# Performance work log

Hardware: AMD Instinct MI355X
Metric: run time of the kernel (lower is better)

The kernel has to match this reference:

```python
import jax, jax.numpy as jnp
import numpy as np

OBS, HID, LAT = 1024, 2048, 256
VOCAB, HQ = 8192, 4
COMMIT = 0.5
N = 16384
LN_EPS = 1e-5


def setup_inputs() -> dict:
    key = jax.random.key(0)
    ks = jax.random.split(key, 7)

    def lin_w(k, fan_in, shape):
        # torch nn.Linear default init: U(-1/sqrt(fan_in), 1/sqrt(fan_in))
        bound = 1.0 / np.sqrt(fan_in)
        return jax.random.uniform(k, shape, jnp.float32, -bound, bound)

    return {
        "x": jax.random.normal(ks[0], (N, OBS), jnp.float32),
        # embeddings initialized uniform(-0.5, 0.5) as in the module
        "codebooks": jax.random.uniform(ks[1], (HQ, VOCAB, LAT), jnp.float32, -0.5, 0.5),
        "enc_w1": lin_w(ks[2], OBS, (OBS, HID)),
        "enc_b1": jnp.zeros((HID,), jnp.float32),
        "ln_g": jnp.ones((HID,), jnp.float32),
        "ln_b": jnp.zeros((HID,), jnp.float32),
        "enc_w2": lin_w(ks[3], HID, (HID, LAT)),
        "enc_b2": jnp.zeros((LAT,), jnp.float32),
        "dec_w1": lin_w(ks[4], LAT, (LAT, HID)),
        "dec_b1": jnp.zeros((HID,), jnp.float32),
        "dec_w2": lin_w(ks[5], HID, (HID, OBS)),
        "dec_b2": jnp.zeros((OBS,), jnp.float32),
    }


def reference(x, codebooks, enc_w1, enc_b1, ln_g, ln_b, enc_w2, enc_b2,
              dec_w1, dec_b1, dec_w2, dec_b2):
    sg = jax.lax.stop_gradient
    # encoder: Linear -> LayerNorm -> ReLU -> Linear
    h = x @ enc_w1 + enc_b1                      # [N, HID]
    mu = h.mean(-1, keepdims=True)
    var = ((h - mu) ** 2).mean(-1, keepdims=True)  # biased var, matches torch LN
    h = (h - mu) * jax.lax.rsqrt(var + LN_EPS) * ln_g + ln_b
    h = jax.nn.relu(h)
    latent = h @ enc_w2 + enc_b2                 # [N, LAT]

    total = jnp.float32(0.0)
    resid = latent
    code_sum = jnp.zeros_like(latent)
    for l in range(HQ):
        E = codebooks[l]                         # [VOCAB, LAT]
        # squared euclidean distances (argmin identical to cdist argmin)
        d2 = ((resid * resid).sum(-1, keepdims=True)
              - 2.0 * (resid @ E.T)
              + (E * E).sum(-1))                 # [N, VOCAB]
        idx = jnp.argmin(d2, axis=-1)            # [N]
        q = E[idx]                               # [N, LAT] gather
        codebook_loss = jnp.mean((q - sg(resid)) ** 2)
        commit_loss = jnp.mean((sg(q) - resid) ** 2)
        total = total + codebook_loss + COMMIT * commit_loss
        code_sum = code_sum + q
        resid = resid - q

    # straight-through estimator
    quant = latent + sg(code_sum - latent)
    # decoder: Linear -> ReLU -> Linear
    dh = jax.nn.relu(quant @ dec_w1 + dec_b1)
    recon = dh @ dec_w2 + dec_b2                 # [N, OBS]
    total = total + 0.5 * jnp.mean((recon - x) ** 2)
    return total
```

## Files before the change

### kernel.cpp

```cpp
#include <hip/hip_runtime.h>

#define N_ROWS 16384
#define OBS    1024
#define HID    2048
#define LAT    256
#define VOCAB  8192
#define HQ     4
#define LN_EPS 1e-5f

typedef unsigned short u16;
typedef unsigned long long u64;
typedef __bf16 bf16x8 __attribute__((ext_vector_type(8)));
typedef float  f32x4  __attribute__((ext_vector_type(4)));

static __device__ __forceinline__ unsigned int float_to_ordered(float f) {
    unsigned int u = __float_as_uint(f);
    return (u & 0x80000000u) ? ~u : (u | 0x80000000u);
}
static __device__ __forceinline__ u16 f2bf(float f) {
    unsigned int u = __float_as_uint(f);
    unsigned int r = u + 0x7FFFu + ((u >> 16) & 1u);
    return (u16)(r >> 16);
}
static __device__ __forceinline__ float bf2f(u16 u) {
    return __uint_as_float((unsigned int)u << 16);
}

#define GL2LDS(gp, lp) __builtin_amdgcn_global_load_lds( \
    (const __attribute__((address_space(1))) void*)(gp), \
    (__attribute__((address_space(3))) void*)(lp), 16, 0, 0)

template<int EPI>
__global__ __launch_bounds__(256, 4) void mfma_gemm_k(
    const u16* __restrict__ Abf, const u16* __restrict__ Bbf,
    const float* __restrict__ bias,
    u16* __restrict__ Cbf,
    float* __restrict__ lat, float* __restrict__ resid, u16* __restrict__ rbf,
    const float* __restrict__ X, double* __restrict__ lacc,
    int K, int Nd)
{
    __shared__ u16 As[128 * 64];
    __shared__ u16 Bs[128 * 64];

    const int tid  = threadIdx.x;
    const int wv   = tid >> 6, lane = tid & 63;
    const int wm   = wv & 1,   wn   = wv >> 1;
    const int m_   = lane & 15, g   = lane >> 4;
    const int m0   = blockIdx.x * 128;
    const int n0   = blockIdx.y * 128;

    f32x4 acc[4][4];
#pragma unroll
    for (int i = 0; i < 4; ++i)
#pragma unroll
        for (int j = 0; j < 4; ++j)
            acc[i][j] = f32x4{0.f, 0.f, 0.f, 0.f};

    const u16* Ablk = Abf + (size_t)m0 * K;
    const u16* Bblk = Bbf + (size_t)n0 * K;

    for (int k0 = 0; k0 < K; k0 += 64) {
#pragma unroll
        for (int c = 0; c < 4; ++c) {
            const int ci = (wv * 4 + c) * 64 + lane;
            const int r  = ci >> 3;
            const int cc = ci & 7;
            const int kc = (cc ^ (r & 7)) << 3;
            GL2LDS(Ablk + (size_t)r * K + k0 + kc, As + (wv * 4 + c) * 512);
            GL2LDS(Bblk + (size_t)r * K + k0 + kc, Bs + (wv * 4 + c) * 512);
        }
        __syncthreads();
#pragma unroll
        for (int ks = 0; ks < 2; ++ks) {
            const int ccw = ks * 4 + g;
            const int sw  = (ccw ^ (m_ & 7)) << 3;
            bf16x8 af[4], bfr[4];
#pragma unroll
            for (int t = 0; t < 4; ++t) {
                af[t]  = *(const bf16x8*)&As[(wm * 64 + t * 16 + m_) * 64 + sw];
                bfr[t] = *(const bf16x8*)&Bs[(wn * 64 + t * 16 + m_) * 64 + sw];
            }
#pragma unroll
            for (int mi = 0; mi < 4; ++mi)
#pragma unroll
                for (int ni = 0; ni < 4; ++ni)
                    acc[mi][ni] = __builtin_amdgcn_mfma_f32_16x16x32_bf16(
                        af[mi], bfr[ni], acc[mi][ni], 0, 0, 0);
        }
        __syncthreads();
    }

    float bs[4];
#pragma unroll
    for (int ni = 0; ni < 4; ++ni) bs[ni] = bias[n0 + wn * 64 + ni * 16 + m_];

    if constexpr (EPI == 3) {
        float lsum = 0.f;
#pragma unroll
        for (int mi = 0; mi < 4; ++mi)
#pragma unroll
            for (int j = 0; j < 4; ++j) {
                const int row = m0 + wm * 64 + mi * 16 + g * 4 + j;
#pragma unroll
                for (int ni = 0; ni < 4; ++ni) {
                    const int col = n0 + wn * 64 + ni * 16 + m_;
                    float r = acc[mi][ni][j] + bs[ni] - X[(size_t)row * Nd + col];
                    lsum = fmaf(r, r, lsum);
                }
            }
#pragma unroll
        for (int off = 32; off >= 1; off >>= 1) lsum += __shfl_xor(lsum, off);
        __shared__ float red[4];
        if (lane == 0) red[wv] = lsum;
        __syncthreads();
        if (tid == 0)
            atomicAdd(lacc, (double)(red[0] + red[1] + red[2] + red[3]));
    } else {
#pragma unroll
        for (int mi = 0; mi < 4; ++mi)
#pragma unroll
            for (int j = 0; j < 4; ++j) {
                const int row = m0 + wm * 64 + mi * 16 + g * 4 + j;
#pragma unroll
                for (int ni = 0; ni < 4; ++ni) {
                    const int col = n0 + wn * 64 + ni * 16 + m_;
                    float v = acc[mi][ni][j] + bs[ni];
                    if constexpr (EPI == 1) v = fmaxf(v, 0.f);
                    if constexpr (EPI == 2) {
                        lat  [(size_t)row * Nd + col] = v;
                        resid[(size_t)row * Nd + col] = v;
                        rbf  [(size_t)row * Nd + col] = f2bf(v);
                    } else {
                        Cbf[(size_t)row * Nd + col] = f2bf(v);
                    }
                }
            }
    }
}

__global__ __launch_bounds__(256) void tpose_bf_k(
    const float* __restrict__ W, u16* __restrict__ Wt, int K, int N)
{
    __shared__ u16 t[32][33];
    const int lx = threadIdx.x & 31, ly = threadIdx.x >> 5;
    const int n0 = blockIdx.x * 32, k0 = blockIdx.y * 32;
#pragma unroll
    for (int i = 0; i < 4; ++i)
        t[ly + 8 * i][lx] = f2bf(W[(size_t)(k0 + ly + 8 * i) * N + n0 + lx]);
    __syncthreads();
#pragma unroll
    for (int i = 0; i < 4; ++i)
        Wt[(size_t)(n0 + ly + 8 * i) * K + k0 + lx] = t[lx][ly + 8 * i];
}

__device__ __forceinline__ float block_reduce_bcast(float v, float* scratch) {
#pragma unroll
    for (int off = 32; off >= 1; off >>= 1) v += __shfl_xor(v, off);
    const int tid = threadIdx.x;
    __syncthreads();
    if ((tid & 63) == 0) scratch[tid >> 6] = v;
    __syncthreads();
    return scratch[0] + scratch[1] + scratch[2] + scratch[3];
}

__global__ __launch_bounds__(256) void ln_relu_bf_k(
    u16* __restrict__ h, const float* __restrict__ g, const float* __restrict__ b)
{
    __shared__ float scratch[4];
    const int tid = threadIdx.x;
    u16* hp = h + (size_t)blockIdx.x * HID + tid * 8;

    ushort4 r0 = *(const ushort4*)hp;
    ushort4 r1 = *(const ushort4*)(hp + 4);
    float v[8] = {bf2f(r0.x), bf2f(r0.y), bf2f(r0.z), bf2f(r0.w),
                  bf2f(r1.x), bf2f(r1.y), bf2f(r1.z), bf2f(r1.w)};

    float s = 0.f;
#pragma unroll
    for (int e = 0; e < 8; ++e) s += v[e];
    const float mu = block_reduce_bcast(s, scratch) * (1.f / HID);

    float vs = 0.f;
#pragma unroll
    for (int e = 0; e < 8; ++e) { float d = v[e] - mu; vs = fmaf(d, d, vs); }
    const float var = block_reduce_bcast(vs, scratch) * (1.f / HID);
    const float rs = rsqrtf(var + LN_EPS);

    ushort4 o0, o1;
#pragma unroll
    for (int e = 0; e < 8; ++e) {
        const int col = tid * 8 + e;
        float w = (v[e] - mu) * rs * g[col] + b[col];
        w = fmaxf(w, 0.f);
        u16 bb = f2bf(w);
        if (e < 4) ((u16*)&o0)[e] = bb; else ((u16*)&o1)[e - 4] = bb;
    }
    *(ushort4*)hp = o0;
    *(ushort4*)(hp + 4) = o1;
}

__global__ __launch_bounds__(256) void enorm_k(
    const float* __restrict__ cb, float* __restrict__ enorm,
    u64* __restrict__ keys, double* __restrict__ accs)
{
    if (blockIdx.x < 64) keys[blockIdx.x * 256 + threadIdx.x] = ~0ull;
    if (blockIdx.x == 64 && threadIdx.x < 2) accs[threadIdx.x] = 0.0;
    const int row  = blockIdx.x * 4 + (threadIdx.x >> 6);
    const int lane = threadIdx.x & 63;
    float4 v = *(const float4*)(cb + (size_t)row * LAT + lane * 4);
    float s = v.x * v.x + v.y * v.y + v.z * v.z + v.w * v.w;
#pragma unroll
    for (int off = 32; off >= 1; off >>= 1) s += __shfl_xor(s, off);
    if (lane == 0) enorm[row] = s;
}

__global__ __launch_bounds__(256) void f2bf_k(
    const float* __restrict__ in, u16* __restrict__ out)
{
    size_t i = ((size_t)blockIdx.x * 256 + threadIdx.x) * 4;
    float4 v = *(const float4*)(in + i);
    ushort4 o;
    o.x = f2bf(v.x); o.y = f2bf(v.y); o.z = f2bf(v.z); o.w = f2bf(v.w);
    *(ushort4*)(out + i) = o;
}

__global__ __launch_bounds__(256) void f2bf_neg2_k(
    const float* __restrict__ in, u16* __restrict__ out)
{
    size_t i = ((size_t)blockIdx.x * 256 + threadIdx.x) * 4;
    float4 v = *(const float4*)(in + i);
    ushort4 o;
    o.x = f2bf(-2.f * v.x); o.y = f2bf(-2.f * v.y);
    o.z = f2bf(-2.f * v.z); o.w = f2bf(-2.f * v.w);
    *(ushort4*)(out + i) = o;
}

__global__ __launch_bounds__(256, 4) void dist_mfma_k(
    const u16* __restrict__ Abf, const u16* __restrict__ Bneg2,
    const float* __restrict__ enorm, u64* __restrict__ keys)
{
    __shared__ u16 As[128 * 64];
    __shared__ u16 Bs[128 * 64];
    __shared__ u64 shk[128][2];

    const int tid  = threadIdx.x;
    const int wv   = tid >> 6, lane = tid & 63;
    const int wm   = wv & 1,   wn   = wv >> 1;
    const int m_   = lane & 15, g   = lane >> 4;
    const int m0   = blockIdx.x * 128;
    const int n0   = blockIdx.y * 128;

    f32x4 acc[4][4];
#pragma unroll
    for (int ni = 0; ni < 4; ++ni) {
        const float en = enorm[n0 + wn * 64 + ni * 16 + m_];
#pragma unroll
        for (int mi = 0; mi < 4; ++mi)
            acc[mi][ni] = f32x4{en, en, en, en};
    }

    const u16* Ablk = Abf   + (size_t)m0 * LAT;
    const u16* Bblk = Bneg2 + (size_t)n0 * LAT;

    for (int k0 = 0; k0 < LAT; k0 += 64) {
#pragma unroll
        for (int c = 0; c < 4; ++c) {
            const int ci = (wv * 4 + c) * 64 + lane;
            const int r  = ci >> 3;
            const int cc = ci & 7;
            const int kc = (cc ^ (r & 7)) << 3;
            GL2LDS(Ablk + (size_t)r * LAT + k0 + kc, As + (wv * 4 + c) * 512);
            GL2LDS(Bblk + (size_t)r * LAT + k0 + kc, Bs + (wv * 4 + c) * 512);
        }
        __syncthreads();
#pragma unroll
        for (int ks = 0; ks < 2; ++ks) {
            const int ccw = ks * 4 + g;
            const int sw  = (ccw ^ (m_ & 7)) << 3;
            bf16x8 af[4], bfr[4];
#pragma unroll
            for (int t = 0; t < 4; ++t) {
                af[t]  = *(const bf16x8*)&As[(wm * 64 + t * 16 + m_) * 64 + sw];
                bfr[t] = *(const bf16x8*)&Bs[(wn * 64 + t * 16 + m_) * 64 + sw];
            }
#pragma unroll
            for (int mi = 0; mi < 4; ++mi)
#pragma unroll
                for (int ni = 0; ni < 4; ++ni)
                    acc[mi][ni] = __builtin_amdgcn_mfma_f32_16x16x32_bf16(
                        af[mi], bfr[ni], acc[mi][ni], 0, 0, 0);
        }
        __syncthreads();
    }

#pragma unroll
    for (int mi = 0; mi < 4; ++mi)
#pragma unroll
        for (int j = 0; j < 4; ++j) {
            float bs_ = acc[mi][0][j];
            int   bi_ = n0 + wn * 64 + m_;
#pragma unroll
            for (int ni = 1; ni < 4; ++ni) {
                const float s = acc[mi][ni][j];
                const int   v = n0 + wn * 64 + ni * 16 + m_;
                if (s < bs_) { bs_ = s; bi_ = v; }
            }
            u64 best = ((u64)float_to_ordered(bs_) << 32) | (unsigned)bi_;
#pragma unroll
            for (int mask = 1; mask <= 8; mask <<= 1) {
                u64 o = __shfl_xor(best, mask);
                best = o < best ? o : best;
            }
            if (m_ == 0) shk[wm * 64 + mi * 16 + g * 4 + j][wn] = best;
        }
    __syncthreads();
    if (tid < 128) {
        u64 a = shk[tid][0], b = shk[tid][1];
        atomicMin(&keys[m0 + tid], a < b ? a : b);
    }
}

template<bool LAST>
__global__ __launch_bounds__(256) void vq_update_k(
    float* __restrict__ resid, u16* __restrict__ aux,
    const float* __restrict__ latent,
    const float* __restrict__ E,
    u64* __restrict__ keys, double* __restrict__ acc)
{
    __shared__ float red[4];
    const int tid = threadIdx.x;
    const int base = blockIdx.x * 16;
    float lsum = 0.f;
    for (int r = 0; r < 16; ++r) {
        const int row = base + r;
        const int idx = (int)(keys[row] & 0xFFFFFFFFull);
        const float q = E[(size_t)idx * LAT + tid];
        float v = resid[(size_t)row * LAT + tid] - q;
        if constexpr (LAST) {
            aux[(size_t)row * LAT + tid] =
                f2bf(latent[(size_t)row * LAT + tid] - v);
        } else {
            resid[(size_t)row * LAT + tid] = v;
            aux[(size_t)row * LAT + tid] = f2bf(v);
        }
        lsum = fmaf(v, v, lsum);
    }
    if (!LAST && tid < 16) keys[base + tid] = ~0ull;
#pragma unroll
    for (int off = 32; off >= 1; off >>= 1) lsum += __shfl_xor(lsum, off);
    if ((tid & 63) == 0) red[tid >> 6] = lsum;
    __syncthreads();
    if (tid == 0) atomicAdd(acc, (double)(red[0] + red[1] + red[2] + red[3]));
}

__global__ void finalize_k(const double* __restrict__ acc, float* __restrict__ out) {
    double total = 1.5 * acc[0] / (double)((size_t)N_ROWS * LAT)
                 + 0.5 * acc[1] / (double)((size_t)N_ROWS * OBS);
    out[0] = (float)total;
}

extern "C" void kernel_launch(void* const* d_in, const int* in_sizes, int n_in,
                              void* d_out, int out_size, void* d_ws, size_t ws_size,
                              hipStream_t stream)
{
    const float* x      = (const float*)d_in[0];
    const float* cb     = (const float*)d_in[1];
    const float* enc_w1 = (const float*)d_in[2];
    const float* enc_b1 = (const float*)d_in[3];
    const float* ln_g   = (const float*)d_in[4];
    const float* ln_b   = (const float*)d_in[5];
    const float* enc_w2 = (const float*)d_in[6];
    const float* enc_b2 = (const float*)d_in[7];
    const float* dec_w1 = (const float*)d_in[8];
    const float* dec_b1 = (const float*)d_in[9];
    const float* dec_w2 = (const float*)d_in[10];
    const float* dec_b2 = (const float*)d_in[11];

    char* ws = (char*)d_ws;
    const size_t MB = 1ull << 20;
    u16* hbuf = (u16*)ws;
    u16* xbf = (u16*)(ws + 64 * MB);
    u16* cbb = (u16*)(ws + 64 * MB);
    u16* rbf = (u16*)(ws + 80 * MB);
    u16* qbf = (u16*)(ws + 88 * MB);
    float* latent = (float*)(ws + 96 * MB);
    float* resid  = (float*)(ws + 112 * MB);
    u16* w1T  = (u16*)(ws + 128 * MB);
    u16* w2T  = (u16*)(ws + 132 * MB);
    u16* wd1T = (u16*)(ws + 133 * MB);
    u16* wd2T = (u16*)(ws + 134 * MB);
    float* enorm = (float*)(ws + 138 * MB);
    u64*   keys  = (u64*)(ws + 138 * MB + 131072);
    double* accs = (double*)(ws + 138 * MB + 262144);

    enorm_k<<<HQ * VOCAB / 4, 256, 0, stream>>>(cb, enorm, keys, accs);

    tpose_bf_k<<<dim3(HID / 32, OBS / 32), 256, 0, stream>>>(enc_w1, w1T, OBS, HID);
    tpose_bf_k<<<dim3(LAT / 32, HID / 32), 256, 0, stream>>>(enc_w2, w2T, HID, LAT);
    tpose_bf_k<<<dim3(HID / 32, LAT / 32), 256, 0, stream>>>(dec_w1, wd1T, LAT, HID);
    tpose_bf_k<<<dim3(OBS / 32, HID / 32), 256, 0, stream>>>(dec_w2, wd2T, HID, OBS);
    f2bf_k<<<(int)((size_t)N_ROWS * OBS / 1024), 256, 0, stream>>>(x, xbf);

    mfma_gemm_k<0><<<dim3(N_ROWS / 128, HID / 128), 256, 0, stream>>>(
        xbf, w1T, enc_b1, hbuf, nullptr, nullptr, nullptr, nullptr, nullptr, OBS, HID);
    ln_relu_bf_k<<<N_ROWS, 256, 0, stream>>>(hbuf, ln_g, ln_b);
    mfma_gemm_k<2><<<dim3(N_ROWS / 128, LAT / 128), 256, 0, stream>>>(
        hbuf, w2T, enc_b2, nullptr, latent, resid, rbf, nullptr, nullptr, HID, LAT);

    f2bf_neg2_k<<<(int)((size_t)HQ * VOCAB * LAT / 1024), 256, 0, stream>>>(cb, cbb);

    for (int l = 0; l < HQ; ++l) {
        dist_mfma_k<<<dim3(N_ROWS / 128, VOCAB / 128), 256, 0, stream>>>(
            rbf, cbb + (size_t)l * VOCAB * LAT, enorm + (size_t)l * VOCAB, keys);
        if (l < HQ - 1)
            vq_update_k<false><<<N_ROWS / 16, 256, 0, stream>>>(
                resid, rbf, nullptr, cb + (size_t)l * VOCAB * LAT, keys, accs);
        else
            vq_update_k<true><<<N_ROWS / 16, 256, 0, stream>>>(
                resid, qbf, latent, cb + (size_t)l * VOCAB * LAT, keys, accs);
    }

    mfma_gemm_k<1><<<dim3(N_ROWS / 128, HID / 128), 256, 0, stream>>>(
        qbf, wd1T, dec_b1, hbuf, nullptr, nullptr, nullptr, nullptr, nullptr, LAT, HID);
    mfma_gemm_k<3><<<dim3(N_ROWS / 128, OBS / 128), 256, 0, stream>>>(
        hbuf, wd2T, dec_b2, nullptr, nullptr, nullptr, nullptr, x, accs + 1, HID, OBS);

    finalize_k<<<1, 1, 0, stream>>>(accs, (float*)d_out);
}
```

Measured before the change: 898.9 us.

## Keep distance A-fragments in registers, double-buffer codebook tiles, retile latent GEMM

```diff
diff --git a/kernel.cpp b/kernel.cpp
--- a/kernel.cpp
+++ b/kernel.cpp
@@ -35,7 +35,6 @@
     const u16* __restrict__ Abf, const u16* __restrict__ Bbf,
     const float* __restrict__ bias,
     u16* __restrict__ Cbf,
-    float* __restrict__ lat, float* __restrict__ resid, u16* __restrict__ rbf,
     const float* __restrict__ X, double* __restrict__ lacc,
     int K, int Nd)
 {
@@ -126,16 +125,82 @@
                     const int col = n0 + wn * 64 + ni * 16 + m_;
                     float v = acc[mi][ni][j] + bs[ni];
                     if constexpr (EPI == 1) v = fmaxf(v, 0.f);
-                    if constexpr (EPI == 2) {
-                        lat  [(size_t)row * Nd + col] = v;
-                        resid[(size_t)row * Nd + col] = v;
-                        rbf  [(size_t)row * Nd + col] = f2bf(v);
-                    } else {
-                        Cbf[(size_t)row * Nd + col] = f2bf(v);
-                    }
+                    Cbf[(size_t)row * Nd + col] = f2bf(v);
                 }
             }
     }
+}
+
+__global__ __launch_bounds__(256, 4) void gemm2_k(
+    const u16* __restrict__ Abf, const u16* __restrict__ Bbf,
+    const float* __restrict__ bias,
+    float* __restrict__ lat, float* __restrict__ resid, u16* __restrict__ rbf)
+{
+    __shared__ u16 As[64 * 64];
+    __shared__ u16 Bs[64 * 64];
+
+    const int tid = threadIdx.x;
+    const int wv  = tid >> 6, lane = tid & 63;
+    const int wm  = wv & 1,   wn   = wv >> 1;
+    const int m_  = lane & 15, g   = lane >> 4;
+    const int m0  = blockIdx.x * 64;
+    const int n0  = blockIdx.y * 64;
+
+    f32x4 acc[2][2];
+#pragma unroll
+    for (int i = 0; i < 2; ++i)
+#pragma unroll
+        for (int j = 0; j < 2; ++j)
+            acc[i][j] = f32x4{0.f, 0.f, 0.f, 0.f};
+
+    const u16* Ablk = Abf + (size_t)m0 * HID;
+    const u16* Bblk = Bbf + (size_t)n0 * HID;
+
+    for (int k0 = 0; k0 < HID; k0 += 64) {
+#pragma unroll
+        for (int c = 0; c < 2; ++c) {
+            const int ci = (wv * 2 + c) * 64 + lane;
+            const int r  = ci >> 3;
+            const int cc = ci & 7;
+            const int kc = (cc ^ (r & 7)) << 3;
+            GL2LDS(Ablk + (size_t)r * HID + k0 + kc, As + (wv * 2 + c) * 512);
+            GL2LDS(Bblk + (size_t)r * HID + k0 + kc, Bs + (wv * 2 + c) * 512);
+        }
+        __syncthreads();
+#pragma unroll
+        for (int ks = 0; ks < 2; ++ks) {
+            const int ccw = ks * 4 + g;
+            const int sw  = (ccw ^ (m_ & 7)) << 3;
+            bf16x8 af[2], bfr[2];
+#pragma unroll
+            for (int t = 0; t < 2; ++t) {
+                af[t]  = *(const bf16x8*)&As[(wm * 32 + t * 16 + m_) * 64 + sw];
+                bfr[t] = *(const bf16x8*)&Bs[(wn * 32 + t * 16 + m_) * 64 + sw];
+            }
+#pragma unroll
+            for (int mi = 0; mi < 2; ++mi)
+#pragma unroll
+                for (int ni = 0; ni < 2; ++ni)
+                    acc[mi][ni] = __builtin_amdgcn_mfma_f32_16x16x32_bf16(
+                        af[mi], bfr[ni], acc[mi][ni], 0, 0, 0);
+        }
+        __syncthreads();
+    }
+
+#pragma unroll
+    for (int mi = 0; mi < 2; ++mi)
+#pragma unroll
+        for (int j = 0; j < 4; ++j) {
+            const int row = m0 + wm * 32 + mi * 16 + g * 4 + j;
+#pragma unroll
+            for (int ni = 0; ni < 2; ++ni) {
+                const int col = n0 + wn * 32 + ni * 16 + m_;
+                float v = acc[mi][ni][j] + bias[col];
+                lat  [(size_t)row * LAT + col] = v;
+                resid[(size_t)row * LAT + col] = v;
+                rbf  [(size_t)row * LAT + col] = f2bf(v);
+            }
+        }
 }
 
 __global__ __launch_bounds__(256) void tpose_bf_k(
@@ -201,16 +266,21 @@
 
 __global__ __launch_bounds__(256) void enorm_k(
     const float* __restrict__ cb, float* __restrict__ enorm,
-    u64* __restrict__ keys, double* __restrict__ accs)
+    u16* __restrict__ cbb, u64* __restrict__ keys, double* __restrict__ accs)
 {
     if (blockIdx.x < 64) keys[blockIdx.x * 256 + threadIdx.x] = ~0ull;
     if (blockIdx.x == 64 && threadIdx.x < 2) accs[threadIdx.x] = 0.0;
     const int row  = blockIdx.x * 4 + (threadIdx.x >> 6);
     const int lane = threadIdx.x & 63;
-    float4 v = *(const float4*)(cb + (size_t)row * LAT + lane * 4);
+    const size_t off = (size_t)row * LAT + lane * 4;
+    float4 v = *(const float4*)(cb + off);
+    ushort4 o;
+    o.x = f2bf(-2.f * v.x); o.y = f2bf(-2.f * v.y);
+    o.z = f2bf(-2.f * v.z); o.w = f2bf(-2.f * v.w);
+    *(ushort4*)(cbb + off) = o;
     float s = v.x * v.x + v.y * v.y + v.z * v.z + v.w * v.w;
 #pragma unroll
-    for (int off = 32; off >= 1; off >>= 1) s += __shfl_xor(s, off);
+    for (int off2 = 32; off2 >= 1; off2 >>= 1) s += __shfl_xor(s, off2);
     if (lane == 0) enorm[row] = s;
 }
 
@@ -224,85 +294,94 @@
     *(ushort4*)(out + i) = o;
 }
 
-__global__ __launch_bounds__(256) void f2bf_neg2_k(
-    const float* __restrict__ in, u16* __restrict__ out)
-{
-    size_t i = ((size_t)blockIdx.x * 256 + threadIdx.x) * 4;
-    float4 v = *(const float4*)(in + i);
-    ushort4 o;
-    o.x = f2bf(-2.f * v.x); o.y = f2bf(-2.f * v.y);
-    o.z = f2bf(-2.f * v.z); o.w = f2bf(-2.f * v.w);
-    *(ushort4*)(out + i) = o;
-}
-
-__global__ __launch_bounds__(256, 4) void dist_mfma_k(
+__global__ __launch_bounds__(256, 3) void dist_mfma_k(
     const u16* __restrict__ Abf, const u16* __restrict__ Bneg2,
     const float* __restrict__ enorm, u64* __restrict__ keys)
 {
-    __shared__ u16 As[128 * 64];
-    __shared__ u16 Bs[128 * 64];
-    __shared__ u64 shk[128][2];
-
-    const int tid  = threadIdx.x;
-    const int wv   = tid >> 6, lane = tid & 63;
-    const int wm   = wv & 1,   wn   = wv >> 1;
-    const int m_   = lane & 15, g   = lane >> 4;
-    const int m0   = blockIdx.x * 128;
-    const int n0   = blockIdx.y * 128;
-
-    f32x4 acc[4][4];
-#pragma unroll
-    for (int ni = 0; ni < 4; ++ni) {
-        const float en = enorm[n0 + wn * 64 + ni * 16 + m_];
-#pragma unroll
-        for (int mi = 0; mi < 4; ++mi)
-            acc[mi][ni] = f32x4{en, en, en, en};
-    }
-
-    const u16* Ablk = Abf   + (size_t)m0 * LAT;
+    __shared__ u16 Bs[2][128 * 64];
+
+    const int tid = threadIdx.x;
+    const int wv  = tid >> 6, lane = tid & 63;
+    const int m_  = lane & 15, g   = lane >> 4;
+    const int m0  = blockIdx.x * 128;
+    const int n0  = blockIdx.y * 128;
+
+    bf16x8 af[2][8];
+    const u16* Arow = Abf + (size_t)(m0 + wv * 32 + m_) * LAT + g * 8;
+#pragma unroll
+    for (int mi = 0; mi < 2; ++mi)
+#pragma unroll
+        for (int kb = 0; kb < 8; ++kb)
+            af[mi][kb] = *(const bf16x8*)(Arow + mi * 16 * LAT + kb * 32);
+
+    f32x4 acc[2][8];
+#pragma unroll
+    for (int ni = 0; ni < 8; ++ni) {
+        const float en = enorm[n0 + ni * 16 + m_];
+        acc[0][ni] = f32x4{en, en, en, en};
+        acc[1][ni] = f32x4{en, en, en, en};
+    }
+
     const u16* Bblk = Bneg2 + (size_t)n0 * LAT;
-
-    for (int k0 = 0; k0 < LAT; k0 += 64) {
-#pragma unroll
-        for (int c = 0; c < 4; ++c) {
-            const int ci = (wv * 4 + c) * 64 + lane;
-            const int r  = ci >> 3;
-            const int cc = ci & 7;
-            const int kc = (cc ^ (r & 7)) << 3;
-            GL2LDS(Ablk + (size_t)r * LAT + k0 + kc, As + (wv * 4 + c) * 512);
-            GL2LDS(Bblk + (size_t)r * LAT + k0 + kc, Bs + (wv * 4 + c) * 512);
-        }
+#pragma unroll
+    for (int c = 0; c < 4; ++c) {
+        const int ci = (wv * 4 + c) * 64 + lane;
+        const int r  = ci >> 3;
+        const int cc = ci & 7;
+        const int kc = (cc ^ (r & 7)) << 3;
+        GL2LDS(Bblk + (size_t)r * LAT + kc, &Bs[0][(wv * 4 + c) * 512]);
+    }
+
+#pragma unroll
+    for (int k0i = 0; k0i < 4; ++k0i) {
         __syncthreads();
+        if (k0i < 3) {
+            const int k0n = (k0i + 1) * 64;
+#pragma unroll
+            for (int c = 0; c < 4; ++c) {
+                const int ci = (wv * 4 + c) * 64 + lane;
+                const int r  = ci >> 3;
+                const int cc = ci & 7;
+                const int kc = (cc ^ (r & 7)) << 3;
+                GL2LDS(Bblk + (size_t)r * LAT + k0n + kc,
+                       &Bs[(k0i + 1) & 1][(wv * 4 + c) * 512]);
+            }
+        }
+        const u16* bsc = Bs[k0i & 1];
 #pragma unroll
         for (int ks = 0; ks < 2; ++ks) {
+            const int kb  = k0i * 2 + ks;
             const int ccw = ks * 4 + g;
             const int sw  = (ccw ^ (m_ & 7)) << 3;
-            bf16x8 af[4], bfr[4];
-#pragma unroll
-            for (int t = 0; t < 4; ++t) {
-                af[t]  = *(const bf16x8*)&As[(wm * 64 + t * 16 + m_) * 64 + sw];
-                bfr[t] = *(const bf16x8*)&Bs[(wn * 64 + t * 16 + m_) * 64 + sw];
-            }
-#pragma unroll
-            for (int mi = 0; mi < 4; ++mi)
-#pragma unroll
-                for (int ni = 0; ni < 4; ++ni)
-                    acc[mi][ni] = __builtin_amdgcn_mfma_f32_16x16x32_bf16(
-                        af[mi], bfr[ni], acc[mi][ni], 0, 0, 0);
-        }
-        __syncthreads();
-    }
-
-#pragma unroll
-    for (int mi = 0; mi < 4; ++mi)
+#pragma unroll
+            for (int nn = 0; nn < 2; ++nn) {
+                bf16x8 bfr[4];
+#pragma unroll
+                for (int q = 0; q < 4; ++q) {
+                    const int row = (nn * 4 + q) * 16 + m_;
+                    bfr[q] = *(const bf16x8*)&bsc[row * 64 + sw];
+                }
+#pragma unroll
+                for (int mi = 0; mi < 2; ++mi)
+#pragma unroll
+                    for (int q = 0; q < 4; ++q)
+                        acc[mi][nn * 4 + q] =
+                            __builtin_amdgcn_mfma_f32_16x16x32_bf16(
+                                af[mi][kb], bfr[q], acc[mi][nn * 4 + q], 0, 0, 0);
+            }
+        }
+    }
+
+#pragma unroll
+    for (int mi = 0; mi < 2; ++mi)
 #pragma unroll
         for (int j = 0; j < 4; ++j) {
             float bs_ = acc[mi][0][j];
-            int   bi_ = n0 + wn * 64 + m_;
-#pragma unroll
-            for (int ni = 1; ni < 4; ++ni) {
+            int   bi_ = n0 + m_;
+#pragma unroll
+            for (int ni = 1; ni < 8; ++ni) {
                 const float s = acc[mi][ni][j];
-                const int   v = n0 + wn * 64 + ni * 16 + m_;
+                const int   v = n0 + ni * 16 + m_;
                 if (s < bs_) { bs_ = s; bi_ = v; }
             }
             u64 best = ((u64)float_to_ordered(bs_) << 32) | (unsigned)bi_;
@@ -311,13 +390,9 @@
                 u64 o = __shfl_xor(best, mask);
                 best = o < best ? o : best;
             }
-            if (m_ == 0) shk[wm * 64 + mi * 16 + g * 4 + j][wn] = best;
-        }
-    __syncthreads();
-    if (tid < 128) {
-        u64 a = shk[tid][0], b = shk[tid][1];
-        atomicMin(&keys[m0 + tid], a < b ? a : b);
-    }
+            if (m_ == 0)
+                atomicMin(&keys[m0 + wv * 32 + mi * 16 + g * 4 + j], best);
+        }
 }
 
 template<bool LAST>
@@ -379,10 +454,10 @@
     char* ws = (char*)d_ws;
     const size_t MB = 1ull << 20;
     u16* hbuf = (u16*)ws;
-    u16* xbf = (u16*)(ws + 64 * MB);
-    u16* cbb = (u16*)(ws + 64 * MB);
-    u16* rbf = (u16*)(ws + 80 * MB);
-    u16* qbf = (u16*)(ws + 88 * MB);
+    u16* cbb  = (u16*)(ws + 64 * MB);
+    u16* rbf  = (u16*)(ws + 80 * MB);
+    u16* qbf  = (u16*)(ws + 88 * MB);
+    u16* xbf  = (u16*)(ws + 96 * MB);
     float* latent = (float*)(ws + 96 * MB);
     float* resid  = (float*)(ws + 112 * MB);
     u16* w1T  = (u16*)(ws + 128 * MB);
@@ -393,7 +468,7 @@
     u64*   keys  = (u64*)(ws + 138 * MB + 131072);
     double* accs = (double*)(ws + 138 * MB + 262144);
 
-    enorm_k<<<HQ * VOCAB / 4, 256, 0, stream>>>(cb, enorm, keys, accs);
+    enorm_k<<<HQ * VOCAB / 4, 256, 0, stream>>>(cb, enorm, cbb, keys, accs);
 
     tpose_bf_k<<<dim3(HID / 32, OBS / 32), 256, 0, stream>>>(enc_w1, w1T, OBS, HID);
     tpose_bf_k<<<dim3(LAT / 32, HID / 32), 256, 0, stream>>>(enc_w2, w2T, HID, LAT);
@@ -402,12 +477,10 @@
     f2bf_k<<<(int)((size_t)N_ROWS * OBS / 1024), 256, 0, stream>>>(x, xbf);
 
     mfma_gemm_k<0><<<dim3(N_ROWS / 128, HID / 128), 256, 0, stream>>>(
-        xbf, w1T, enc_b1, hbuf, nullptr, nullptr, nullptr, nullptr, nullptr, OBS, HID);
+        xbf, w1T, enc_b1, hbuf, nullptr, nullptr, OBS, HID);
     ln_relu_bf_k<<<N_ROWS, 256, 0, stream>>>(hbuf, ln_g, ln_b);
-    mfma_gemm_k<2><<<dim3(N_ROWS / 128, LAT / 128), 256, 0, stream>>>(
-        hbuf, w2T, enc_b2, nullptr, latent, resid, rbf, nullptr, nullptr, HID, LAT);
-
-    f2bf_neg2_k<<<(int)((size_t)HQ * VOCAB * LAT / 1024), 256, 0, stream>>>(cb, cbb);
+    gemm2_k<<<dim3(N_ROWS / 64, LAT / 64), 256, 0, stream>>>(
+        hbuf, w2T, enc_b2, latent, resid, rbf);
 
     for (int l = 0; l < HQ; ++l) {
         dist_mfma_k<<<dim3(N_ROWS / 128, VOCAB / 128), 256, 0, stream>>>(
@@ -421,9 +494,9 @@
     }
 
     mfma_gemm_k<1><<<dim3(N_ROWS / 128, HID / 128), 256, 0, stream>>>(
-        qbf, wd1T, dec_b1, hbuf, nullptr, nullptr, nullptr, nullptr, nullptr, LAT, HID);
+        qbf, wd1T, dec_b1, hbuf, nullptr, nullptr, LAT, HID);
     mfma_gemm_k<3><<<dim3(N_ROWS / 128, OBS / 128), 256, 0, stream>>>(
-        hbuf, wd2T, dec_b2, nullptr, nullptr, nullptr, nullptr, x, accs + 1, HID, OBS);
+        hbuf, wd2T, dec_b2, nullptr, x, accs + 1, HID, OBS);
 
     finalize_k<<<1, 1, 0, stream>>>(accs, (float*)d_out);
 }
```

Result: slower. 923.1 us (+2.7%).
